# Kernel optimization log

Hardware: AMD Instinct MI355X
Metric: run time of the kernel (lower is better)

Reference implementation:

```python
import jax, jax.numpy as jnp
import numpy as np

N = 50000      # nodes
E = 800000     # edges
D = 128        # node feature dim
H = 128        # hid_channel (hardcoded in module)
B = 64         # graphs in batch
C = 3          # num_classes (COLLAB)
K = N // 2     # TopKPooling ratio=0.5


def setup_inputs() -> dict:
    key = jax.random.key(0)
    ks = jax.random.split(key, 16)
    s = 0.05
    return {
        "x": jax.random.normal(ks[0], (N, D), dtype=jnp.float32),
        "edge_index": jax.random.randint(ks[1], (E, 2), 0, N),
        "batch": jnp.sort(jax.random.randint(ks[2], (N,), 0, B)),
        "W1": jax.random.normal(ks[3], (D, H), dtype=jnp.float32) * s,
        "b1": jnp.zeros((H,), jnp.float32),
        "W2": jax.random.normal(ks[4], (H, H), dtype=jnp.float32) * s,
        "b2": jnp.zeros((H,), jnp.float32),
        "p": jax.random.normal(ks[5], (H,), dtype=jnp.float32),
        "W3": jax.random.normal(ks[6], (H, H), dtype=jnp.float32) * s,
        "b3": jnp.zeros((H,), jnp.float32),
        "W4": jax.random.normal(ks[7], (H, H), dtype=jnp.float32) * s,
        "b4": jnp.zeros((H,), jnp.float32),
        "fcW1": jax.random.normal(ks[8], (H, H), dtype=jnp.float32) * s,
        "fcb1": jnp.zeros((H,), jnp.float32),
        "fcW2": jax.random.normal(ks[9], (H, C), dtype=jnp.float32) * s,
        "fcb2": jnp.zeros((C,), jnp.float32),
    }


def gcn_conv(x, src, dst, ew, W, b, n):
    # PyG GCNConv: D^{-1/2}(A+I)D^{-1/2} x W + b, deg includes self-loop
    h = x @ W
    deg = jax.ops.segment_sum(ew, dst, num_segments=n) + 1.0
    dinv = jax.lax.rsqrt(deg)
    coef = dinv[src] * dinv[dst] * ew            # [E]
    agg = jax.ops.segment_sum(coef[:, None] * h[src], dst, num_segments=n)
    return agg + (dinv * dinv)[:, None] * h + b  # self-loop term + bias


def reference(x, edge_index, batch, W1, b1, W2, b2, p, W3, b3, W4, b4, fcW1, fcb1, fcW2, fcb2):
    src, dst = edge_index[:, 0], edge_index[:, 1]
    ew = jnp.ones((E,), x.dtype)

    h = jax.nn.relu(gcn_conv(x, src, dst, ew, W1, b1, N))
    h = jax.nn.relu(gcn_conv(h, src, dst, ew, W2, b2, N))

    # TopKPooling: score = x.p/||p||, keep top K, gate by tanh(score)
    score = h @ p / jnp.linalg.norm(p)
    top_vals, perm = jax.lax.top_k(score, K)
    hp = h[perm] * jnp.tanh(top_vals)[:, None]
    batch_p = batch[perm]
    new_idx = jnp.full((N,), -1, jnp.int32).at[perm].set(jnp.arange(K, dtype=jnp.int32))
    ns, nd = new_idx[src], new_idx[dst]
    mask = (ns >= 0) & (nd >= 0)
    ewp = mask.astype(x.dtype)
    ns = jnp.where(mask, ns, 0)
    nd = jnp.where(mask, nd, 0)

    h = jax.nn.relu(gcn_conv(hp, ns, nd, ewp, W3, b3, K))
    h = jax.nn.relu(gcn_conv(h, ns, nd, ewp, W4, b4, K))

    # global mean pool over graphs
    sums = jax.ops.segment_sum(h, batch_p, num_segments=B)
    cnt = jax.ops.segment_sum(jnp.ones((K,), x.dtype), batch_p, num_segments=B)
    g = sums / jnp.maximum(cnt, 1.0)[:, None]

    g = jax.nn.relu(g @ fcW1 + fcb1)
    logits = g @ fcW2 + fcb2
    return jax.nn.log_softmax(logits, axis=1)
```

## Files before the change

### kernel.cpp

```cpp
#include <hip/hip_runtime.h>

#define N_NODES 50000
#define N_EDGES 800000
#define HDIM    128
#define NBATCH  64
#define NCLS    3
#define KSEL    (N_NODES/2)
#define MMB_ROWS 64
#define HIST_BLOCKS 128
#define POOL_BLOCKS 256
#define POOL_CHUNK  ((KSEL + POOL_BLOCKS - 1) / POOL_BLOCKS)

typedef unsigned long long u64;
typedef unsigned int u32;
typedef unsigned short ushort_t;
typedef _Float16 half8 __attribute__((ext_vector_type(8)));
typedef float floatx4 __attribute__((ext_vector_type(4)));

struct SelState { u64 prefix; int krem; int cnt; };

__device__ __forceinline__ float h2f(ushort_t u) {
    _Float16 h = *(_Float16*)&u;
    return (float)h;
}

__global__ void init_state_k(SelState* st) {
    st->prefix = 0ull; st->krem = KSEL; st->cnt = 0;
}

__global__ void deg_full_k(const int* __restrict__ ei, int* __restrict__ degi) {
    int e = blockIdx.x * blockDim.x + threadIdx.x;
    if (e >= N_EDGES) return;
    atomicAdd(&degi[ei[2*e+1]], 1);
}

__global__ void deg_pool_k(const int* __restrict__ ei, const int* __restrict__ o2n,
        int* __restrict__ degi) {
    int e = blockIdx.x * blockDim.x + threadIdx.x;
    if (e >= N_EDGES) return;
    int ns = o2n[ei[2*e]], nd = o2n[ei[2*e+1]];
    if (ns >= 0 && nd >= 0) atomicAdd(&degi[nd], 1);
}

__global__ __launch_bounds__(256) void scan1_k(const int* __restrict__ degi,
        int* __restrict__ bsum, float* __restrict__ dinv, int n) {
    __shared__ int sh[256];
    int t = threadIdx.x;
    int i = blockIdx.x * 256 + t;
    int d = (i < n) ? degi[i] : 0;
    if (i < n) dinv[i] = rsqrtf((float)d + 1.0f);
    sh[t] = d;
    __syncthreads();
    for (int s = 128; s > 0; s >>= 1) {
        if (t < s) sh[t] += sh[t + s];
        __syncthreads();
    }
    if (t == 0) bsum[blockIdx.x] = sh[0];
}

__global__ __launch_bounds__(256) void scan2_k(const int* __restrict__ bsum,
        int* __restrict__ boff, int* __restrict__ rowptr, int nb, int n) {
    __shared__ int sh[256];
    int t = threadIdx.x;
    int v = (t < nb) ? bsum[t] : 0;
    sh[t] = v;
    __syncthreads();
    for (int d = 1; d < 256; d <<= 1) {
        int u = (t >= d) ? sh[t - d] : 0;
        __syncthreads();
        sh[t] += u;
        __syncthreads();
    }
    if (t < nb) boff[t] = sh[t] - v;
    if (t == 255) rowptr[n] = sh[255];
}

__global__ __launch_bounds__(256) void scan3_k(const int* __restrict__ degi,
        const int* __restrict__ boff, int* __restrict__ rowptr, int n) {
    __shared__ int sh[256];
    int t = threadIdx.x;
    int i = blockIdx.x * 256 + t;
    int v = (i < n) ? degi[i] : 0;
    sh[t] = v;
    __syncthreads();
    for (int d = 1; d < 256; d <<= 1) {
        int u = (t >= d) ? sh[t - d] : 0;
        __syncthreads();
        sh[t] += u;
        __syncthreads();
    }
    if (i < n) rowptr[i] = boff[blockIdx.x] + sh[t] - v;
}

__global__ void fill_csr_k(const int* __restrict__ ei, const int* __restrict__ rowptr,
        int* __restrict__ fillcnt, int* __restrict__ csr) {
    int e = blockIdx.x * blockDim.x + threadIdx.x;
    if (e >= N_EDGES) return;
    int d = ei[2*e+1];
    int pos = rowptr[d] + atomicAdd(&fillcnt[d], 1);
    csr[pos] = ei[2*e];
}

__global__ void fill_csr_pool_k(const int* __restrict__ ei, const int* __restrict__ o2n,
        const int* __restrict__ rowptr, int* __restrict__ fillcnt, int* __restrict__ csr) {
    int e = blockIdx.x * blockDim.x + threadIdx.x;
    if (e >= N_EDGES) return;
    int ns = o2n[ei[2*e]], nd = o2n[ei[2*e+1]];
    if (ns < 0 || nd < 0) return;
    int pos = rowptr[nd] + atomicAdd(&fillcnt[nd], 1);
    csr[pos] = ns;
}

__global__ __launch_bounds__(256) void gather_k(const int* __restrict__ rowptr,
        const int* __restrict__ csr, const float* __restrict__ dinv,
        const ushort_t* __restrict__ hb, const float* __restrict__ bias,
        float* __restrict__ out, int n) {
    int node = blockIdx.x * 4 + (threadIdx.x >> 6);
    if (node >= n) return;
    int lane = threadIdx.x & 63;
    float di = dinv[node];
    float2 bv = *(const float2*)&bias[2*lane];
    ushort2 hs = *(const ushort2*)&hb[(size_t)node * HDIM + 2*lane];
    float s2 = di * di;
    float accx = s2 * h2f(hs.x) + bv.x;
    float accy = s2 * h2f(hs.y) + bv.y;
    int rs = rowptr[node], re = rowptr[node + 1];
    for (int base = rs; base < re; base += 64) {
        int cnt = min(64, re - base);
        int srcv = 0; float cv = 0.0f;
        if (lane < cnt) { srcv = csr[base + lane]; cv = di * dinv[srcv]; }
        int j = 0;
        for (; j + 8 <= cnt; j += 8) {
            int s0 = __shfl(srcv, j+0, 64); int s1 = __shfl(srcv, j+1, 64);
            int s2i= __shfl(srcv, j+2, 64); int s3 = __shfl(srcv, j+3, 64);
            int s4 = __shfl(srcv, j+4, 64); int s5 = __shfl(srcv, j+5, 64);
            int s6 = __shfl(srcv, j+6, 64); int s7 = __shfl(srcv, j+7, 64);
            float c0 = __shfl(cv, j+0, 64); float c1 = __shfl(cv, j+1, 64);
            float c2 = __shfl(cv, j+2, 64); float c3 = __shfl(cv, j+3, 64);
            float c4 = __shfl(cv, j+4, 64); float c5 = __shfl(cv, j+5, 64);
            float c6 = __shfl(cv, j+6, 64); float c7 = __shfl(cv, j+7, 64);
            ushort2 v0 = *(const ushort2*)&hb[(size_t)s0 * HDIM + 2*lane];
            ushort2 v1 = *(const ushort2*)&hb[(size_t)s1 * HDIM + 2*lane];
            ushort2 v2 = *(const ushort2*)&hb[(size_t)s2i* HDIM + 2*lane];
            ushort2 v3 = *(const ushort2*)&hb[(size_t)s3 * HDIM + 2*lane];
            ushort2 v4 = *(const ushort2*)&hb[(size_t)s4 * HDIM + 2*lane];
            ushort2 v5 = *(const ushort2*)&hb[(size_t)s5 * HDIM + 2*lane];
            ushort2 v6 = *(const ushort2*)&hb[(size_t)s6 * HDIM + 2*lane];
            ushort2 v7 = *(const ushort2*)&hb[(size_t)s7 * HDIM + 2*lane];
            accx += c0*h2f(v0.x); accy += c0*h2f(v0.y);
            accx += c1*h2f(v1.x); accy += c1*h2f(v1.y);
            accx += c2*h2f(v2.x); accy += c2*h2f(v2.y);
            accx += c3*h2f(v3.x); accy += c3*h2f(v3.y);
            accx += c4*h2f(v4.x); accy += c4*h2f(v4.y);
            accx += c5*h2f(v5.x); accy += c5*h2f(v5.y);
            accx += c6*h2f(v6.x); accy += c6*h2f(v6.y);
            accx += c7*h2f(v7.x); accy += c7*h2f(v7.y);
        }
        for (; j < cnt; ++j) {
            int src = __shfl(srcv, j, 64);
            float c  = __shfl(cv, j, 64);
            ushort2 sv = *(const ushort2*)&hb[(size_t)src * HDIM + 2*lane];
            accx += c * h2f(sv.x);
            accy += c * h2f(sv.y);
        }
    }
    float2 o; o.x = accx; o.y = accy;
    *(float2*)&out[(size_t)node * HDIM + 2*lane] = o;
}

__global__ void pnorm_k(const float* __restrict__ p, float* __restrict__ pn) {
    __shared__ float red[HDIM];
    int t = threadIdx.x;
    float v = p[t];
    red[t] = v * v;
    __syncthreads();
    for (int s = HDIM/2; s > 0; s >>= 1) {
        if (t < s) red[t] += red[t+s];
        __syncthreads();
    }
    pn[t] = v / sqrtf(red[0]);
}

template<bool RELU_IN>
__global__ __launch_bounds__(256) void matmul_k(const float* __restrict__ in,
        const float* __restrict__ W, ushort_t* __restrict__ outb, int rows) {
    __shared__ _Float16 Wf[4][8][64][8];
    int t = threadIdx.x;
    int rbase = blockIdx.x * MMB_ROWS;
    for (int idx = t; idx < HDIM * HDIM; idx += 256) {
        int k = idx >> 7, j = idx & 127;
        int kk = k >> 5, kgrp = (k >> 3) & 3, i = k & 7;
        int ct = j >> 4, lrow = j & 15;
        Wf[kk][ct][kgrp * 16 + lrow][i] = (_Float16)W[idx];
    }
    int wid = t >> 6, lane = t & 63;
    int lrow = lane & 15, kgrp = lane >> 4;
    int arow = rbase + wid * 16 + lrow;
    bool rowok = (arow < rows);
    const float* arp = in + (size_t)(rowok ? arow : 0) * HDIM + kgrp * 8;
    half8 a[4];
#pragma unroll
    for (int kk = 0; kk < 4; ++kk) {
        float4 lo = rowok ? *(const float4*)(arp + kk * 32)     : float4{0,0,0,0};
        float4 hi = rowok ? *(const float4*)(arp + kk * 32 + 4) : float4{0,0,0,0};
        if (RELU_IN) {
            lo.x = fmaxf(lo.x, 0.f); lo.y = fmaxf(lo.y, 0.f);
            lo.z = fmaxf(lo.z, 0.f); lo.w = fmaxf(lo.w, 0.f);
            hi.x = fmaxf(hi.x, 0.f); hi.y = fmaxf(hi.y, 0.f);
            hi.z = fmaxf(hi.z, 0.f); hi.w = fmaxf(hi.w, 0.f);
        }
        a[kk][0] = (_Float16)lo.x; a[kk][1] = (_Float16)lo.y;
        a[kk][2] = (_Float16)lo.z; a[kk][3] = (_Float16)lo.w;
        a[kk][4] = (_Float16)hi.x; a[kk][5] = (_Float16)hi.y;
        a[kk][6] = (_Float16)hi.z; a[kk][7] = (_Float16)hi.w;
    }
    __syncthreads();
    floatx4 zero4 = {0.0f, 0.0f, 0.0f, 0.0f};
    floatx4 acc[8];
#pragma unroll
    for (int ct = 0; ct < 8; ++ct) acc[ct] = zero4;
#pragma unroll
    for (int kk = 0; kk < 4; ++kk) {
#pragma unroll
        for (int ct = 0; ct < 8; ++ct) {
            half8 b = *(const half8*)&Wf[kk][ct][lane][0];
            acc[ct] = __builtin_amdgcn_mfma_f32_16x16x32_f16(a[kk], b, acc[ct], 0, 0, 0);
        }
    }
    int orow0 = rbase + wid * 16 + kgrp * 4;
#pragma unroll
    for (int ct = 0; ct < 8; ++ct) {
#pragma unroll
        for (int i = 0; i < 4; ++i) {
            int row = orow0 + i;
            if (row < rows) {
                _Float16 hv = (_Float16)acc[ct][i];
                outb[(size_t)row * HDIM + ct * 16 + lrow] = *(ushort_t*)&hv;
            }
        }
    }
}

__global__ void score_key_k(const float* __restrict__ h, const float* __restrict__ pn,
        float* __restrict__ score, u64* __restrict__ key) {
    int gid  = blockIdx.x * blockDim.x + threadIdx.x;
    int node = gid >> 6;
    int lane = gid & 63;
    if (node >= N_NODES) return;
    const float* row = h + (size_t)node * HDIM;
    float sv = fmaxf(row[lane], 0.f) * pn[lane] + fmaxf(row[lane+64], 0.f) * pn[lane+64];
#pragma unroll
    for (int o = 32; o > 0; o >>= 1) sv += __shfl_xor(sv, o, 64);
    if (lane == 0) {
        score[node] = sv;
        u32 u = __float_as_uint(sv);
        u = (u & 0x80000000u) ? ~u : (u | 0x80000000u);
        key[node] = ((u64)u << 16) | (u64)(65535 - node);
    }
}

__global__ __launch_bounds__(256) void hist_k(const u64* __restrict__ key,
        const SelState* __restrict__ st, u32* __restrict__ hist, int pass) {
    __shared__ u32 lh[256];
    int t = threadIdx.x;
    lh[t] = 0;
    __syncthreads();
    int dsh = 40 - 8 * pass;
    u64 pref = st->prefix;
    for (int i = blockIdx.x * 256 + t; i < N_NODES; i += HIST_BLOCKS * 256) {
        u64 k = key[i];
        if (((k ^ pref) >> (dsh + 8)) == 0)
            atomicAdd(&lh[(int)((k >> dsh) & 255)], 1u);
    }
    __syncthreads();
    u32 v = lh[t];
    if (v) atomicAdd(&hist[pass * 256 + t], v);
}

__global__ void scan_k(const u32* __restrict__ hist, SelState* st, int pass) {
    __shared__ u32 c[256];
    int t = threadIdx.x;
    c[t] = hist[pass * 256 + t];
    __syncthreads();
    if (t == 0) {
        int dsh = 40 - 8 * pass;
        int krem = st->krem;
        int b = 255;
        for (; b > 0; --b) {
            int cnt = (int)c[b];
            if (cnt < krem) krem -= cnt;
            else break;
        }
        st->prefix |= ((u64)b) << dsh;
        st->krem = krem;
    }
}

__global__ void select_k(const u64* __restrict__ key, SelState* st,
        int* __restrict__ o2n, int* __restrict__ n2o) {
    int i = blockIdx.x * blockDim.x + threadIdx.x;
    if (i >= N_NODES) return;
    if (key[i] >= st->prefix) {
        int pos = atomicAdd(&st->cnt, 1);
        o2n[i] = pos;
        n2o[pos] = i;
    } else {
        o2n[i] = -1;
    }
}

__global__ void hp_k(const float* __restrict__ h2, const float* __restrict__ score,
        const int* __restrict__ n2o, float* __restrict__ hp) {
    int gid = blockIdx.x * blockDim.x + threadIdx.x;
    if (gid >= KSEL * 32) return;
    int k  = gid >> 5;
    int c4 = (gid & 31) << 2;
    int old = n2o[k];
    float tv = tanhf(score[old]);
    float4 hv = *(const float4*)&h2[(size_t)old * HDIM + c4];
    float4 o;
    o.x = fmaxf(hv.x, 0.f) * tv;
    o.y = fmaxf(hv.y, 0.f) * tv;
    o.z = fmaxf(hv.z, 0.f) * tv;
    o.w = fmaxf(hv.w, 0.f) * tv;
    *(float4*)&hp[(size_t)k * HDIM + c4] = o;
}

__global__ __launch_bounds__(256) void pool_stage1_k(const float* __restrict__ h,
        const int* __restrict__ n2o, const int* __restrict__ batch,
        float* __restrict__ partial, int* __restrict__ pcnt) {
    __shared__ float ls[NBATCH * HDIM];
    __shared__ int   lc[NBATCH];
    int t = threadIdx.x;
    for (int i = t; i < NBATCH * HDIM; i += 256) ls[i] = 0.0f;
    if (t < NBATCH) lc[t] = 0;
    __syncthreads();
    int wid = t >> 6, lane = t & 63;
    int start = blockIdx.x * POOL_CHUNK;
    int end = min(start + POOL_CHUNK, KSEL);
    for (int k = start + wid; k < end; k += 4) {
        int b = batch[n2o[k]];
        float2 hv = *(const float2*)&h[(size_t)k * HDIM + 2*lane];
        atomicAdd(&ls[b * HDIM + 2*lane],     fmaxf(hv.x, 0.0f));
        atomicAdd(&ls[b * HDIM + 2*lane + 1], fmaxf(hv.y, 0.0f));
        if (lane == 0) atomicAdd(&lc[b], 1);
    }
    __syncthreads();
    float* pb = partial + (size_t)blockIdx.x * (NBATCH * HDIM);
    for (int i = t; i < NBATCH * HDIM; i += 256) pb[i] = ls[i];
    if (t < NBATCH) pcnt[blockIdx.x * NBATCH + t] = lc[t];
}

__global__ __launch_bounds__(256) void pool_stage2_k(const float* __restrict__ partial,
        const int* __restrict__ pcnt, float* __restrict__ sums, float* __restrict__ cntb) {
    int i = blockIdx.x * 256 + threadIdx.x;
    if (i >= NBATCH * HDIM) return;
    float s = 0.0f;
    for (int p = 0; p < POOL_BLOCKS; ++p) s += partial[(size_t)p * NBATCH * HDIM + i];
    sums[i] = s;
    if (i < NBATCH) {
        int c = 0;
        for (int p = 0; p < POOL_BLOCKS; ++p) c += pcnt[p * NBATCH + i];
        cntb[i] = (float)c;
    }
}

__global__ void fc1_k(const float* __restrict__ sums, const float* __restrict__ cntb,
        const float* __restrict__ W, const float* __restrict__ bias, float* __restrict__ g) {
    int gid = blockIdx.x * blockDim.x + threadIdx.x;
    if (gid >= NBATCH * HDIM) return;
    int b = gid >> 7, j = gid & 127;
    float inv = 1.0f / fmaxf(cntb[b], 1.0f);
    float acc = 0.0f;
    for (int k = 0; k < HDIM; ++k) acc += sums[b * HDIM + k] * W[k * HDIM + j];
    acc = acc * inv + bias[j];
    g[gid] = fmaxf(acc, 0.0f);
}

__global__ void fc2_k(const float* __restrict__ g, const float* __restrict__ W,
        const float* __restrict__ bias, float* __restrict__ out) {
    int b = threadIdx.x;
    if (b >= NBATCH) return;
    float l[NCLS];
    for (int c = 0; c < NCLS; ++c) {
        float acc = bias[c];
        for (int k = 0; k < HDIM; ++k) acc += g[b * HDIM + k] * W[k * NCLS + c];
        l[c] = acc;
    }
    float m = fmaxf(l[0], fmaxf(l[1], l[2]));
    float sum = expf(l[0]-m) + expf(l[1]-m) + expf(l[2]-m);
    float ls = logf(sum);
    for (int c = 0; c < NCLS; ++c) out[b * NCLS + c] = l[c] - m - ls;
}

extern "C" void kernel_launch(void* const* d_in, const int* in_sizes, int n_in,
                              void* d_out, int out_size, void* d_ws, size_t ws_size,
                              hipStream_t stream) {
    const float* x    = (const float*)d_in[0];
    const int*   ei   = (const int*)d_in[1];
    const int*   batch= (const int*)d_in[2];
    const float* W1   = (const float*)d_in[3];
    const float* b1   = (const float*)d_in[4];
    const float* W2   = (const float*)d_in[5];
    const float* b2   = (const float*)d_in[6];
    const float* p    = (const float*)d_in[7];
    const float* W3   = (const float*)d_in[8];
    const float* b3   = (const float*)d_in[9];
    const float* W4   = (const float*)d_in[10];
    const float* b4   = (const float*)d_in[11];
    const float* fcW1 = (const float*)d_in[12];
    const float* fcb1 = (const float*)d_in[13];
    const float* fcW2 = (const float*)d_in[14];
    const float* fcb2 = (const float*)d_in[15];
    float* out = (float*)d_out;

    char* ws = (char*)d_ws;
    size_t off = 0;
    auto alloc = [&](size_t bytes) {
        size_t r = off;
        off = (off + bytes + 255) & ~(size_t)255;
        return r;
    };
    float* A     = (float*)(ws + alloc((size_t)N_NODES * HDIM * 4));
    float* Bf    = (float*)(ws + alloc((size_t)N_NODES * HDIM * 4));
    ushort_t* Hbf= (ushort_t*)(ws + alloc((size_t)N_NODES * HDIM * 2));
    u64*   key   = (u64*)  (ws + alloc((size_t)N_NODES * 8));
    float* score = (float*)(ws + alloc((size_t)N_NODES * 4));
    int*   o2n   = (int*)  (ws + alloc((size_t)N_NODES * 4));
    int*   n2o   = (int*)  (ws + alloc((size_t)KSEL * 4));
    float* pn    = (float*)(ws + alloc(HDIM * 4));
    float* gbuf  = (float*)(ws + alloc(NBATCH * HDIM * 4));
    SelState* st = (SelState*)(ws + alloc(256));
    float* dinv1 = (float*)(ws + alloc((size_t)N_NODES * 4));
    float* dinvp = (float*)(ws + alloc((size_t)KSEL * 4));
    int*   rowptr= (int*)  (ws + alloc((size_t)(N_NODES + 1) * 4));
    int*   csr   = (int*)  (ws + alloc((size_t)N_EDGES * 4));
    int*   bsum  = (int*)  (ws + alloc(256 * 4));
    int*   boff  = (int*)  (ws + alloc(256 * 4));
    float* partial=(float*)(ws + alloc((size_t)POOL_BLOCKS * NBATCH * HDIM * 4));
    int*   pcnt  = (int*)  (ws + alloc((size_t)POOL_BLOCKS * NBATCH * 4));
    float* sums  = (float*)(ws + alloc(NBATCH * HDIM * 4));
    float* cntb  = (float*)(ws + alloc(NBATCH * 4));
    size_t z1 = off;
    int*   degi   = (int*)(ws + alloc((size_t)N_NODES * 4));
    int*   fillcnt= (int*)(ws + alloc((size_t)N_NODES * 4));
    size_t z1e = off;
    size_t z2 = off;
    u32*   hist  = (u32*)  (ws + alloc(6 * 256 * 4));
    size_t z2e = off;

    hipMemsetAsync(ws + z1, 0, z2e - z1, stream);
    init_state_k<<<1, 1, 0, stream>>>(st);
    pnorm_k<<<1, HDIM, 0, stream>>>(p, pn);

    const int eg   = (N_EDGES + 255) / 256;
    const int ng   = (N_NODES + 255) / 256;
    const int kg   = (KSEL + 255) / 256;
    const int mm_grid_n = (N_NODES + MMB_ROWS - 1) / MMB_ROWS;
    const int mm_grid_k = (KSEL + MMB_ROWS - 1) / MMB_ROWS;
    const int gt_grid_n = (N_NODES + 3) / 4;
    const int gt_grid_k = (KSEL + 3) / 4;
    const int kh4_grid  = (KSEL * 32 + 255) / 256;

    deg_full_k<<<eg, 256, 0, stream>>>(ei, degi);
    scan1_k<<<ng, 256, 0, stream>>>(degi, bsum, dinv1, N_NODES);
    scan2_k<<<1, 256, 0, stream>>>(bsum, boff, rowptr, ng, N_NODES);
    scan3_k<<<ng, 256, 0, stream>>>(degi, boff, rowptr, N_NODES);
    fill_csr_k<<<eg, 256, 0, stream>>>(ei, rowptr, fillcnt, csr);

    matmul_k<false><<<mm_grid_n, 256, 0, stream>>>(x, W1, Hbf, N_NODES);
    gather_k<<<gt_grid_n, 256, 0, stream>>>(rowptr, csr, dinv1, Hbf, b1, Bf, N_NODES);
    matmul_k<true><<<mm_grid_n, 256, 0, stream>>>(Bf, W2, Hbf, N_NODES);
    gather_k<<<gt_grid_n, 256, 0, stream>>>(rowptr, csr, dinv1, Hbf, b2, Bf, N_NODES);

    score_key_k<<<(N_NODES * 64 + 255) / 256, 256, 0, stream>>>(Bf, pn, score, key);
    for (int pass = 0; pass < 6; ++pass) {
        hist_k<<<HIST_BLOCKS, 256, 0, stream>>>(key, st, hist, pass);
        scan_k<<<1, 256, 0, stream>>>(hist, st, pass);
    }
    select_k<<<ng, 256, 0, stream>>>(key, st, o2n, n2o);
    hp_k<<<kh4_grid, 256, 0, stream>>>(Bf, score, n2o, A);

    hipMemsetAsync(ws + z1, 0, z1e - z1, stream);
    deg_pool_k<<<eg, 256, 0, stream>>>(ei, o2n, degi);
    scan1_k<<<kg, 256, 0, stream>>>(degi, bsum, dinvp, KSEL);
    scan2_k<<<1, 256, 0, stream>>>(bsum, boff, rowptr, kg, KSEL);
    scan3_k<<<kg, 256, 0, stream>>>(degi, boff, rowptr, KSEL);
    fill_csr_pool_k<<<eg, 256, 0, stream>>>(ei, o2n, rowptr, fillcnt, csr);

    matmul_k<false><<<mm_grid_k, 256, 0, stream>>>(A, W3, Hbf, KSEL);
    gather_k<<<gt_grid_k, 256, 0, stream>>>(rowptr, csr, dinvp, Hbf, b3, Bf, KSEL);
    matmul_k<true><<<mm_grid_k, 256, 0, stream>>>(Bf, W4, Hbf, KSEL);
    gather_k<<<gt_grid_k, 256, 0, stream>>>(rowptr, csr, dinvp, Hbf, b4, A, KSEL);

    pool_stage1_k<<<POOL_BLOCKS, 256, 0, stream>>>(A, n2o, batch, partial, pcnt);
    pool_stage2_k<<<(NBATCH * HDIM + 255) / 256, 256, 0, stream>>>(partial, pcnt, sums, cntb);
    fc1_k<<<(NBATCH * HDIM + 255) / 256, 256, 0, stream>>>(sums, cntb, fcW1, fcb1, gbuf);
    fc2_k<<<1, 64, 0, stream>>>(gbuf, fcW2, fcb2, out);
}
```

Baseline: 432.0 us.

## Build pooled CSR from full CSR and fuse scans via last-block pattern

Builds the pooled graph's CSR by walking each kept node's row in the existing full CSR, using wavefront ballots to count and compact surviving neighbours. This replaces the edge-wise atomic degree and fill passes over all edges with o2n lookups. It also merges scan1/scan2 and hist/scan into single kernels using a last-block-done counter, merges init with pnorm, and uses int2 edge loads. This cuts kernel launches and atomics but adds workspace buffers and relies on threadfence-based cross-block handoff.

```diff
diff --git a/kernel.cpp b/kernel.cpp
--- a/kernel.cpp
+++ b/kernel.cpp
@@ -24,27 +24,33 @@
     return (float)h;
 }
 
-__global__ void init_state_k(SelState* st) {
-    st->prefix = 0ull; st->krem = KSEL; st->cnt = 0;
+__global__ void init_pnorm_k(const float* __restrict__ p, float* __restrict__ pn,
+        SelState* st) {
+    __shared__ float red[HDIM];
+    int t = threadIdx.x;
+    float v = p[t];
+    red[t] = v * v;
+    __syncthreads();
+    for (int s = HDIM/2; s > 0; s >>= 1) {
+        if (t < s) red[t] += red[t+s];
+        __syncthreads();
+    }
+    pn[t] = v / sqrtf(red[0]);
+    if (t == 0) { st->prefix = 0ull; st->krem = KSEL; st->cnt = 0; }
 }
 
 __global__ void deg_full_k(const int* __restrict__ ei, int* __restrict__ degi) {
     int e = blockIdx.x * blockDim.x + threadIdx.x;
     if (e >= N_EDGES) return;
-    atomicAdd(&degi[ei[2*e+1]], 1);
-}
-
-__global__ void deg_pool_k(const int* __restrict__ ei, const int* __restrict__ o2n,
-        int* __restrict__ degi) {
-    int e = blockIdx.x * blockDim.x + threadIdx.x;
-    if (e >= N_EDGES) return;
-    int ns = o2n[ei[2*e]], nd = o2n[ei[2*e+1]];
-    if (ns >= 0 && nd >= 0) atomicAdd(&degi[nd], 1);
-}
-
-__global__ __launch_bounds__(256) void scan1_k(const int* __restrict__ degi,
-        int* __restrict__ bsum, float* __restrict__ dinv, int n) {
+    int2 ed = ((const int2*)ei)[e];
+    atomicAdd(&degi[ed.y], 1);
+}
+
+__global__ __launch_bounds__(256) void scan12_k(const int* __restrict__ degi,
+        int* __restrict__ bsum, int* __restrict__ boff, float* __restrict__ dinv,
+        int* __restrict__ rowptr, int n, int nb, int* done) {
     __shared__ int sh[256];
+    __shared__ int lastf;
     int t = threadIdx.x;
     int i = blockIdx.x * 256 + t;
     int d = (i < n) ? degi[i] : 0;
@@ -55,24 +61,26 @@
         if (t < s) sh[t] += sh[t + s];
         __syncthreads();
     }
-    if (t == 0) bsum[blockIdx.x] = sh[0];
-}
-
-__global__ __launch_bounds__(256) void scan2_k(const int* __restrict__ bsum,
-        int* __restrict__ boff, int* __restrict__ rowptr, int nb, int n) {
-    __shared__ int sh[256];
-    int t = threadIdx.x;
-    int v = (t < nb) ? bsum[t] : 0;
-    sh[t] = v;
-    __syncthreads();
-    for (int d = 1; d < 256; d <<= 1) {
-        int u = (t >= d) ? sh[t - d] : 0;
+    if (t == 0) {
+        atomicExch(&bsum[blockIdx.x], sh[0]);
+        __threadfence();
+        int dd = atomicAdd(done, 1);
+        lastf = (dd == (int)gridDim.x - 1) ? 1 : 0;
+    }
+    __syncthreads();
+    if (lastf) {
+        int v = (t < nb) ? atomicAdd(&bsum[t], 0) : 0;
+        sh[t] = v;
         __syncthreads();
-        sh[t] += u;
-        __syncthreads();
-    }
-    if (t < nb) boff[t] = sh[t] - v;
-    if (t == 255) rowptr[n] = sh[255];
+        for (int dl = 1; dl < 256; dl <<= 1) {
+            int u = (t >= dl) ? sh[t - dl] : 0;
+            __syncthreads();
+            sh[t] += u;
+            __syncthreads();
+        }
+        if (t < nb) boff[t] = sh[t] - v;
+        if (t == 255) rowptr[n] = sh[255];
+    }
 }
 
 __global__ __launch_bounds__(256) void scan3_k(const int* __restrict__ degi,
@@ -96,19 +104,50 @@
         int* __restrict__ fillcnt, int* __restrict__ csr) {
     int e = blockIdx.x * blockDim.x + threadIdx.x;
     if (e >= N_EDGES) return;
-    int d = ei[2*e+1];
-    int pos = rowptr[d] + atomicAdd(&fillcnt[d], 1);
-    csr[pos] = ei[2*e];
-}
-
-__global__ void fill_csr_pool_k(const int* __restrict__ ei, const int* __restrict__ o2n,
-        const int* __restrict__ rowptr, int* __restrict__ fillcnt, int* __restrict__ csr) {
-    int e = blockIdx.x * blockDim.x + threadIdx.x;
-    if (e >= N_EDGES) return;
-    int ns = o2n[ei[2*e]], nd = o2n[ei[2*e+1]];
-    if (ns < 0 || nd < 0) return;
-    int pos = rowptr[nd] + atomicAdd(&fillcnt[nd], 1);
-    csr[pos] = ns;
+    int2 ed = ((const int2*)ei)[e];
+    int pos = rowptr[ed.y] + atomicAdd(&fillcnt[ed.y], 1);
+    csr[pos] = ed.x;
+}
+
+__global__ __launch_bounds__(256) void pool_deg_k(const int* __restrict__ rowptr,
+        const int* __restrict__ csr, const int* __restrict__ n2o,
+        const int* __restrict__ o2n, int* __restrict__ degp) {
+    int k = blockIdx.x * 4 + (threadIdx.x >> 6);
+    if (k >= KSEL) return;
+    int lane = threadIdx.x & 63;
+    int old = n2o[k];
+    int rs = rowptr[old], re = rowptr[old + 1];
+    int cnt = 0;
+    for (int base = rs; base < re; base += 64) {
+        int span = min(64, re - base);
+        bool sel = false;
+        if (lane < span) sel = (o2n[csr[base + lane]] >= 0);
+        u64 m = __ballot(sel);
+        cnt += __popcll(m);
+    }
+    if (lane == 0) degp[k] = cnt;
+}
+
+__global__ __launch_bounds__(256) void pool_fill_k(const int* __restrict__ rowptr,
+        const int* __restrict__ csr, const int* __restrict__ n2o,
+        const int* __restrict__ o2n, const int* __restrict__ rowptrp,
+        int* __restrict__ csrp) {
+    int k = blockIdx.x * 4 + (threadIdx.x >> 6);
+    if (k >= KSEL) return;
+    int lane = threadIdx.x & 63;
+    int old = n2o[k];
+    int rs = rowptr[old], re = rowptr[old + 1];
+    int wpos = rowptrp[k];
+    for (int base = rs; base < re; base += 64) {
+        int span = min(64, re - base);
+        int ns = -1;
+        if (lane < span) ns = o2n[csr[base + lane]];
+        bool sel = (ns >= 0);
+        u64 m = __ballot(sel);
+        int off = __popcll(m & ((1ull << lane) - 1ull));
+        if (sel) csrp[wpos + off] = ns;
+        wpos += __popcll(m);
+    }
 }
 
 __global__ __launch_bounds__(256) void gather_k(const int* __restrict__ rowptr,
@@ -168,19 +207,6 @@
     *(float2*)&out[(size_t)node * HDIM + 2*lane] = o;
 }
 
-__global__ void pnorm_k(const float* __restrict__ p, float* __restrict__ pn) {
-    __shared__ float red[HDIM];
-    int t = threadIdx.x;
-    float v = p[t];
-    red[t] = v * v;
-    __syncthreads();
-    for (int s = HDIM/2; s > 0; s >>= 1) {
-        if (t < s) red[t] += red[t+s];
-        __syncthreads();
-    }
-    pn[t] = v / sqrtf(red[0]);
-}
-
 template<bool RELU_IN>
 __global__ __launch_bounds__(256) void matmul_k(const float* __restrict__ in,
         const float* __restrict__ W, ushort_t* __restrict__ outb, int rows) {
@@ -259,9 +285,10 @@
     }
 }
 
-__global__ __launch_bounds__(256) void hist_k(const u64* __restrict__ key,
-        const SelState* __restrict__ st, u32* __restrict__ hist, int pass) {
+__global__ __launch_bounds__(256) void histscan_k(const u64* __restrict__ key,
+        SelState* st, u32* __restrict__ hist, int pass, int* done) {
     __shared__ u32 lh[256];
+    __shared__ int lastf;
     int t = threadIdx.x;
     lh[t] = 0;
     __syncthreads();
@@ -275,24 +302,27 @@
     __syncthreads();
     u32 v = lh[t];
     if (v) atomicAdd(&hist[pass * 256 + t], v);
-}
-
-__global__ void scan_k(const u32* __restrict__ hist, SelState* st, int pass) {
-    __shared__ u32 c[256];
-    int t = threadIdx.x;
-    c[t] = hist[pass * 256 + t];
+    __threadfence();
     __syncthreads();
     if (t == 0) {
-        int dsh = 40 - 8 * pass;
-        int krem = st->krem;
-        int b = 255;
-        for (; b > 0; --b) {
-            int cnt = (int)c[b];
-            if (cnt < krem) krem -= cnt;
-            else break;
-        }
-        st->prefix |= ((u64)b) << dsh;
-        st->krem = krem;
+        int dd = atomicAdd(done, 1);
+        lastf = (dd == HIST_BLOCKS - 1) ? 1 : 0;
+    }
+    __syncthreads();
+    if (lastf) {
+        lh[t] = atomicAdd(&hist[pass * 256 + t], 0u);
+        __syncthreads();
+        if (t == 0) {
+            int krem = st->krem;
+            int b = 255;
+            for (; b > 0; --b) {
+                int cnt = (int)lh[b];
+                if (cnt < krem) krem -= cnt;
+                else break;
+            }
+            st->prefix |= ((u64)b) << dsh;
+            st->krem = krem;
+        }
     }
 }
 
@@ -435,6 +465,9 @@
     float* dinvp = (float*)(ws + alloc((size_t)KSEL * 4));
     int*   rowptr= (int*)  (ws + alloc((size_t)(N_NODES + 1) * 4));
     int*   csr   = (int*)  (ws + alloc((size_t)N_EDGES * 4));
+    int*   rowptrp=(int*)  (ws + alloc((size_t)(KSEL + 1) * 4));
+    int*   csrp  = (int*)  (ws + alloc((size_t)N_EDGES * 4));
+    int*   degp  = (int*)  (ws + alloc((size_t)KSEL * 4));
     int*   bsum  = (int*)  (ws + alloc(256 * 4));
     int*   boff  = (int*)  (ws + alloc(256 * 4));
     float* partial=(float*)(ws + alloc((size_t)POOL_BLOCKS * NBATCH * HDIM * 4));
@@ -444,14 +477,12 @@
     size_t z1 = off;
     int*   degi   = (int*)(ws + alloc((size_t)N_NODES * 4));
     int*   fillcnt= (int*)(ws + alloc((size_t)N_NODES * 4));
+    u32*   hist  = (u32*)  (ws + alloc(6 * 256 * 4));
+    int*   done  = (int*)  (ws + alloc(16 * 4));
     size_t z1e = off;
-    size_t z2 = off;
-    u32*   hist  = (u32*)  (ws + alloc(6 * 256 * 4));
-    size_t z2e = off;
-
-    hipMemsetAsync(ws + z1, 0, z2e - z1, stream);
-    init_state_k<<<1, 1, 0, stream>>>(st);
-    pnorm_k<<<1, HDIM, 0, stream>>>(p, pn);
+
+    hipMemsetAsync(ws + z1, 0, z1e - z1, stream);
+    init_pnorm_k<<<1, HDIM, 0, stream>>>(p, pn, st);
 
     const int eg   = (N_EDGES + 255) / 256;
     const int ng   = (N_NODES + 255) / 256;
@@ -463,8 +494,7 @@
     const int kh4_grid  = (KSEL * 32 + 255) / 256;
 
     deg_full_k<<<eg, 256, 0, stream>>>(ei, degi);
-    scan1_k<<<ng, 256, 0, stream>>>(degi, bsum, dinv1, N_NODES);
-    scan2_k<<<1, 256, 0, stream>>>(bsum, boff, rowptr, ng, N_NODES);
+    scan12_k<<<ng, 256, 0, stream>>>(degi, bsum, boff, dinv1, rowptr, N_NODES, ng, done + 0);
     scan3_k<<<ng, 256, 0, stream>>>(degi, boff, rowptr, N_NODES);
     fill_csr_k<<<eg, 256, 0, stream>>>(ei, rowptr, fillcnt, csr);
 
@@ -474,24 +504,20 @@
     gather_k<<<gt_grid_n, 256, 0, stream>>>(rowptr, csr, dinv1, Hbf, b2, Bf, N_NODES);
 
     score_key_k<<<(N_NODES * 64 + 255) / 256, 256, 0, stream>>>(Bf, pn, score, key);
-    for (int pass = 0; pass < 6; ++pass) {
-        hist_k<<<HIST_BLOCKS, 256, 0, stream>>>(key, st, hist, pass);
-        scan_k<<<1, 256, 0, stream>>>(hist, st, pass);
-    }
+    for (int pass = 0; pass < 6; ++pass)
+        histscan_k<<<HIST_BLOCKS, 256, 0, stream>>>(key, st, hist, pass, done + 2 + pass);
     select_k<<<ng, 256, 0, stream>>>(key, st, o2n, n2o);
     hp_k<<<kh4_grid, 256, 0, stream>>>(Bf, score, n2o, A);
 
-    hipMemsetAsync(ws + z1, 0, z1e - z1, stream);
-    deg_pool_k<<<eg, 256, 0, stream>>>(ei, o2n, degi);
-    scan1_k<<<kg, 256, 0, stream>>>(degi, bsum, dinvp, KSEL);
-    scan2_k<<<1, 256, 0, stream>>>(bsum, boff, rowptr, kg, KSEL);
-    scan3_k<<<kg, 256, 0, stream>>>(degi, boff, rowptr, KSEL);
-    fill_csr_pool_k<<<eg, 256, 0, stream>>>(ei, o2n, rowptr, fillcnt, csr);
+    pool_deg_k<<<gt_grid_k, 256, 0, stream>>>(rowptr, csr, n2o, o2n, degp);
+    scan12_k<<<kg, 256, 0, stream>>>(degp, bsum, boff, dinvp, rowptrp, KSEL, kg, done + 1);
+    scan3_k<<<kg, 256, 0, stream>>>(degp, boff, rowptrp, KSEL);
+    pool_fill_k<<<gt_grid_k, 256, 0, stream>>>(rowptr, csr, n2o, o2n, rowptrp, csrp);
 
     matmul_k<false><<<mm_grid_k, 256, 0, stream>>>(A, W3, Hbf, KSEL);
-    gather_k<<<gt_grid_k, 256, 0, stream>>>(rowptr, csr, dinvp, Hbf, b3, Bf, KSEL);
+    gather_k<<<gt_grid_k, 256, 0, stream>>>(rowptrp, csrp, dinvp, Hbf, b3, Bf, KSEL);
     matmul_k<true><<<mm_grid_k, 256, 0, stream>>>(Bf, W4, Hbf, KSEL);
-    gather_k<<<gt_grid_k, 256, 0, stream>>>(rowptr, csr, dinvp, Hbf, b4, A, KSEL);
+    gather_k<<<gt_grid_k, 256, 0, stream>>>(rowptrp, csrp, dinvp, Hbf, b4, A, KSEL);
 
     pool_stage1_k<<<POOL_BLOCKS, 256, 0, stream>>>(A, n2o, batch, partial, pcnt);
     pool_stage2_k<<<(NBATCH * HDIM + 255) / 256, 256, 0, stream>>>(partial, pcnt, sums, cntb);
```

Measured after the change: 451.0 us. 1.04x slower.
